# Kernel optimization log

Measured on AMD Instinct MI355X. Metric: run time of the kernel, lower is better.

## Reference

```python
import jax, jax.numpy as jnp
import numpy as np

LRELU_ALPHA = 0.2   # LeakyReLU negative slope (alpha init arg)
NEG_INF = -9e15     # masking constant used by standard GAT layers

B, N, NFEAT, NHID, NHEAD, NPRED = 16, 1024, 16, 32, 4, 12


def setup_inputs() -> dict:
    key = jax.random.key(0)
    ks = jax.random.split(key, 8)
    x = jax.random.normal(ks[0], (B, N, NFEAT), dtype=jnp.float32)
    adj = jax.random.randint(ks[1], (N, N), 0, 2, dtype=jnp.int32)
    s = 0.1
    W = jax.random.normal(ks[2], (NHEAD, NFEAT, NHID), dtype=jnp.float32) * s
    a_src = jax.random.normal(ks[3], (NHEAD, NHID), dtype=jnp.float32) * s
    a_dst = jax.random.normal(ks[4], (NHEAD, NHID), dtype=jnp.float32) * s
    W_out = jax.random.normal(ks[5], (NHEAD * NHID, NPRED), dtype=jnp.float32) * s
    a_out_src = jax.random.normal(ks[6], (NPRED,), dtype=jnp.float32) * s
    a_out_dst = jax.random.normal(ks[7], (NPRED,), dtype=jnp.float32) * s
    return {"x": x, "adj": adj, "W": W, "a_src": a_src, "a_dst": a_dst,
            "W_out": W_out, "a_out_src": a_out_src, "a_out_dst": a_out_dst}


def reference(x, adj, W, a_src, a_dst, W_out, a_out_src, a_out_dst):
    # Eval mode: all F.dropout calls are identity.
    mask = adj > 0  # [N, N], broadcast over batch (and heads)

    # --- multi-head GAT layer (concat=True), all heads vectorized ---
    Wh = jnp.einsum('bnf,hfk->bhnk', x, W)                 # [B,H,N,K]
    f_src = jnp.einsum('bhnk,hk->bhn', Wh, a_src)          # [B,H,N]
    f_dst = jnp.einsum('bhnk,hk->bhn', Wh, a_dst)
    e = jax.nn.leaky_relu(f_src[..., :, None] + f_dst[..., None, :], LRELU_ALPHA)
    attn = jax.nn.softmax(jnp.where(mask, e, NEG_INF), axis=-1)  # [B,H,N,N]
    h = jax.nn.elu(jnp.einsum('bhnm,bhmk->bhnk', attn, Wh))      # concat=True -> ELU
    b, H, n, k = h.shape
    h = jnp.transpose(h, (0, 2, 1, 3)).reshape(b, n, H * k)  # concat heads, dim=2

    # --- output GAT layer (concat=False) ---
    Wh2 = h @ W_out                                        # [B,N,npred]
    g_src = Wh2 @ a_out_src                                # [B,N]
    g_dst = Wh2 @ a_out_dst
    e2 = jax.nn.leaky_relu(g_src[:, :, None] + g_dst[:, None, :], LRELU_ALPHA)
    attn2 = jax.nn.softmax(jnp.where(mask, e2, NEG_INF), axis=-1)
    out = jax.nn.elu(jnp.einsum('bnm,bmp->bnp', attn2, Wh2))  # outer F.elu in STGAT
    return out.reshape(b, -1)                              # [B, N*npred]
```

## Files before the change

kernel.cpp:

```cpp
#include <hip/hip_runtime.h>
#include <cmath>

#define B_    16
#define N_    1024
#define NHID_ 32
#define NHEAD_ 4
#define NPRED_ 12
#define ALPHA 0.2f
#define LOG2E 1.442695041f

typedef __attribute__((ext_vector_type(8)))  short          short8;
typedef __attribute__((ext_vector_type(4)))  float          floatx4;
typedef __attribute__((ext_vector_type(2)))  float          float2v;
typedef __attribute__((ext_vector_type(4)))  unsigned       uintx4;
typedef __attribute__((ext_vector_type(4)))  unsigned short ushort4v;
typedef __attribute__((ext_vector_type(8)))  unsigned short ushort8v;

__device__ __forceinline__ float bs2f(unsigned short s) {
    return __uint_as_float(((unsigned)s) << 16);
}
__device__ __forceinline__ short f2bs(float f) {
    unsigned u = __float_as_uint(f);
    unsigned r = (u + 0x7fffu + ((u >> 16) & 1u)) >> 16;
    return (short)r;
}
__device__ __forceinline__ float ldin(const void* p, long i, int isbf) {
    if (isbf) return bs2f(((const unsigned short*)p)[i]);
    return ((const float*)p)[i];
}
__device__ __forceinline__ float fexp2(float x) {
#if __has_builtin(__builtin_amdgcn_exp2f)
    return __builtin_amdgcn_exp2f(x);
#else
    return __expf(x * 0.6931471805599453f);
#endif
}
__device__ __forceinline__ unsigned pk2t(unsigned u0, unsigned u1) {
#if __has_builtin(__builtin_amdgcn_perm)
    return __builtin_amdgcn_perm(u1, u0, 0x07060302u);
#else
    return (u0 >> 16) | (u1 & 0xffff0000u);
#endif
}
__device__ __forceinline__ float2v vmax2(float2v a, float2v b) {
#if __has_builtin(__builtin_elementwise_max)
    return __builtin_elementwise_max(a, b);
#else
    float2v r; r.x = fmaxf(a.x, b.x); r.y = fmaxf(a.y, b.y); return r;
#endif
}
__device__ __forceinline__ float2v vfma2(float2v a, float2v b, float2v c) {
#if __has_builtin(__builtin_elementwise_fma)
    return __builtin_elementwise_fma(a, b, c);
#else
    float2v r; r.x = __builtin_fmaf(a.x, b.x, c.x); r.y = __builtin_fmaf(a.y, b.y, c.y); return r;
#endif
}
__device__ __forceinline__ int detect_isbf(const unsigned short* xu) {
    int lane = threadIdx.x & 63;
    uint4 v = ((const uint4*)xu)[lane];
    unsigned wv[4] = {v.x, v.y, v.z, v.w};
    bool any = false;
#pragma unroll
    for (int i = 0; i < 4; ++i) {
        any |= (((wv[i] & 0xffffu) >> 7) & 0xffu) >= 160u;
        any |= (((wv[i] >> 16) >> 7) & 0xffu) >= 160u;
    }
    return __popcll(__ballot(any)) < 8;
}

__global__ __launch_bounds__(256) void k01_prep_wh(
    const unsigned short* __restrict__ xu, const int* __restrict__ adj,
    const void* __restrict__ x, const void* __restrict__ W,
    const void* __restrict__ a_src, const void* __restrict__ a_dst,
    unsigned short* __restrict__ bias,
    short* __restrict__ WhB, float* __restrict__ f_src, float* __restrict__ f_dst)
{
    int tid = threadIdx.x;
    if (blockIdx.x < 512) {
        int gid = blockIdx.x * 256 + tid;
        long base = (long)gid * 8;
        int4 a0 = *(const int4*)(adj + base);
        int4 a1 = *(const int4*)(adj + base + 4);
        uint4 wv;
        wv.x = (a0.x ? 0u : 0xFF80u) | (a0.y ? 0u : 0xFF800000u);
        wv.y = (a0.z ? 0u : 0xFF80u) | (a0.w ? 0u : 0xFF800000u);
        wv.z = (a1.x ? 0u : 0xFF80u) | (a1.y ? 0u : 0xFF800000u);
        wv.w = (a1.z ? 0u : 0xFF80u) | (a1.w ? 0u : 0xFF800000u);
        *(uint4*)(bias + base) = wv;
        return;
    }
    int isbf = detect_isbf(xu);
    __shared__ float Ws[16][32];
    __shared__ float xs[32][17];
    __shared__ float as_s[32], ad_s[32];
    __shared__ float Wa_s[16], Wad_s[16];
    int bid = blockIdx.x - 512;
    int bh = bid >> 5;
    int n0 = (bid & 31) * 32;
    int b  = bh >> 2, hh = bh & 3;

    if (!isbf) {
        const float* Wf = (const float*)W + hh * 512;
        if (tid < 128) {
            float4 v = *(const float4*)(Wf + tid * 4);
            int f = (tid * 4) >> 5, k = (tid * 4) & 31;
            Ws[f][k] = v.x; Ws[f][k+1] = v.y; Ws[f][k+2] = v.z; Ws[f][k+3] = v.w;
        }
        const float* xf = (const float*)x + ((long)(b * N_ + n0)) * 16;
        if (tid < 128) {
            float4 v = *(const float4*)(xf + tid * 4);
            int r = tid >> 2, f = (tid & 3) * 4;
            xs[r][f] = v.x; xs[r][f+1] = v.y; xs[r][f+2] = v.z; xs[r][f+3] = v.w;
        }
    } else {
        const unsigned short* Wb = (const unsigned short*)W + hh * 512;
        if (tid < 128) {
            ushort4v v = *(const ushort4v*)(Wb + tid * 4);
            int f = (tid * 4) >> 5, k = (tid * 4) & 31;
            Ws[f][k] = bs2f(v[0]); Ws[f][k+1] = bs2f(v[1]);
            Ws[f][k+2] = bs2f(v[2]); Ws[f][k+3] = bs2f(v[3]);
        }
        const unsigned short* xb = (const unsigned short*)x + ((long)(b * N_ + n0)) * 16;
        if (tid < 64) {
            ushort8v v = *(const ushort8v*)(xb + tid * 8);
            int r = tid >> 1, f = (tid & 1) * 8;
#pragma unroll
            for (int i = 0; i < 8; ++i) xs[r][f + i] = bs2f(v[i]);
        }
    }
    if (tid < 32) {
        as_s[tid] = ldin(a_src, hh * 32 + tid, isbf);
        ad_s[tid] = ldin(a_dst, hh * 32 + tid, isbf);
    }
    __syncthreads();

    if (tid < 32) {
        int f = tid & 15;
        const float* av = (tid < 16) ? as_s : ad_s;
        float s = 0.f;
#pragma unroll
        for (int kk = 0; kk < 32; ++kk) s += Ws[f][kk] * av[kk];
        ((tid < 16) ? Wa_s : Wad_s)[f] = s;
    }
    __syncthreads();

    if (tid < 32) {
        float fs = 0.f, fd = 0.f;
#pragma unroll
        for (int f = 0; f < 16; ++f) {
            fs += xs[tid][f] * Wa_s[f];
            fd += xs[tid][f] * Wad_s[f];
        }
        int n = n0 + tid;
        f_src[bh * N_ + n] = fs * LOG2E;
        f_dst[bh * N_ + n] = fd * LOG2E;
    }

    int k = tid & 31, rb = tid >> 5;
#pragma unroll
    for (int it = 0; it < 4; ++it) {
        int r = it * 8 + rb;
        float acc = 0.f;
#pragma unroll
        for (int f = 0; f < 16; ++f) acc += xs[r][f] * Ws[f][k];
        int n = n0 + r;
        int kstep = n >> 5, quad = (n >> 3) & 3, jj = n & 7;
        int t = k >> 4, l = quad * 16 + (k & 15);
        WhB[((((size_t)bh * 32 + kstep) * 2 + t) * 64 + l) * 8 + jj] = f2bs(acc);
    }
}

__global__ __launch_bounds__(256) void k2_attn1(
    const float* __restrict__ f_src, const float* __restrict__ f_dst,
    const unsigned short* __restrict__ bias, const short* __restrict__ WhB,
    unsigned short* __restrict__ h2)
{
    __shared__ float fdst_s[N_];
    __shared__ float wmax[4];
    __shared__ float Sh[4][16];
    int bid = blockIdx.x;
    int xcd = bid & 7, j = bid >> 3;
    int bh = j & 63;
    int tile = xcd + 8 * (j >> 6);
    int tid = threadIdx.x;
    int w = tid >> 6, lane = tid & 63;

    float lmax = -INFINITY;
    for (int idx = tid; idx < N_; idx += 256) {
        float v = f_dst[bh * N_ + idx];
        fdst_s[idx] = v;
        lmax = fmaxf(lmax, v);
    }
#pragma unroll
    for (int m = 32; m; m >>= 1) lmax = fmaxf(lmax, __shfl_xor(lmax, m, 64));
    if (lane == 0) wmax[w] = lmax;
    __syncthreads();
    float maxfd = fmaxf(fmaxf(wmax[0], wmax[1]), fmaxf(wmax[2], wmax[3]));

    int i0 = tile * 64 + w * 16;
    int r = lane & 15, q = lane >> 4;

    float fsr = f_src[bh * N_ + i0 + r];
    float Mv = fsr + maxfd;
    float M = fmaxf(Mv, ALPHA * Mv);
    float2v a1v; a1v.x = fsr - M;          a1v.y = a1v.x;
    float2v a2v; a2v.x = ALPHA * fsr - M;  a2v.y = a2v.x;
    float2v alv; alv.x = ALPHA;            alv.y = ALPHA;
    float2v s2 = {};

    floatx4 acc0 = {}, acc1 = {};
    const unsigned short* brow = bias + (size_t)(i0 + r) * N_ + q * 8;
    const float* fdp = fdst_s + q * 8;
    const short* wb = WhB + (((size_t)bh * 64) * 64 + lane) * 8;

    uint4  bu_n = *(const uint4*)(brow);
    short8 w0_n = *(const short8*)(wb);
    short8 w1_n = *(const short8*)(wb + 512);

#pragma unroll 4
    for (int kk = 0; kk < 32; ++kk) {
        uint4 bu = bu_n;
        short8 bfr0 = w0_n, bfr1 = w1_n;
        if (kk < 31) {
            bu_n = *(const uint4*)(brow + (kk + 1) * 32);
            w0_n = *(const short8*)(wb + (kk + 1) * 1024);
            w1_n = *(const short8*)(wb + (kk + 1) * 1024 + 512);
        }
        float4 fda = *(const float4*)(fdp + kk * 32);
        float4 fdb = *(const float4*)(fdp + kk * 32 + 4);
        unsigned bw[4] = {bu.x, bu.y, bu.z, bu.w};
        float fdx[8] = {fda.x, fda.y, fda.z, fda.w, fdb.x, fdb.y, fdb.z, fdb.w};
        unsigned dpk[4];
#pragma unroll
        for (int p = 0; p < 4; ++p) {
            float2v fd2; fd2.x = fdx[2 * p]; fd2.y = fdx[2 * p + 1];
            float2v b2;  b2.x = __uint_as_float(bw[p] << 16);
                         b2.y = __uint_as_float(bw[p] & 0xffff0000u);
            float2v t1 = a1v + fd2;
            float2v t2 = vfma2(alv, fd2, a2v);
            float2v arg = vmax2(t1, t2) + b2;
            float2v pv; pv.x = fexp2(arg.x); pv.y = fexp2(arg.y);
            s2 += pv;
            dpk[p] = pk2t(__float_as_uint(pv.x), __float_as_uint(pv.y));
        }
        uintx4 du; du[0] = dpk[0]; du[1] = dpk[1]; du[2] = dpk[2]; du[3] = dpk[3];
        short8 afr = __builtin_bit_cast(short8, du);
        acc0 = __builtin_amdgcn_mfma_f32_16x16x32_bf16(afr, bfr0, acc0, 0, 0, 0);
        acc1 = __builtin_amdgcn_mfma_f32_16x16x32_bf16(afr, bfr1, acc1, 0, 0, 0);
    }

    float s = s2.x + s2.y;
    s += __shfl_xor(s, 16, 64);
    s += __shfl_xor(s, 32, 64);
    if (lane < 16) Sh[w][lane] = s;
    __builtin_amdgcn_wave_barrier();

    int bb = bh >> 2, head = bh & 3;
#pragma unroll
    for (int reg = 0; reg < 4; ++reg) {
        int row = q * 4 + reg;
        float rsv = 1.f / Sh[w][row];
        unsigned short* hrow = &h2[((size_t)(bb * N_ + i0 + row)) * 128 + head * 32];
        float v0 = acc0[reg] * rsv;
        v0 = v0 > 0.f ? v0 : expm1f(v0);
        hrow[r]      = (unsigned short)f2bs(v0);
        float v1 = acc1[reg] * rsv;
        v1 = v1 > 0.f ? v1 : expm1f(v1);
        hrow[16 + r] = (unsigned short)f2bs(v1);
    }
}

__global__ __launch_bounds__(256) void k3_out_proj(
    const unsigned short* __restrict__ xu,
    const unsigned short* __restrict__ h2, const void* __restrict__ W_out,
    const void* __restrict__ a_out_src, const void* __restrict__ a_out_dst,
    short* __restrict__ Wh2B, float* __restrict__ g_src, float* __restrict__ g_dst)
{
    int isbf = detect_isbf(xu);
    __shared__ float WoT[16][132];
    __shared__ float hs[16][132];
    __shared__ float aos[16], aod[16];
    int bid = blockIdx.x;
    int b = bid >> 6;
    int n0 = (bid & 63) * 16;
    int tid = threadIdx.x;

    if (!isbf) {
        const float* Wf = (const float*)W_out;
        for (int idx = tid; idx < 384; idx += 256) {
            float4 v = *(const float4*)(Wf + idx * 4);
            float vv[4] = {v.x, v.y, v.z, v.w};
#pragma unroll
            for (int i = 0; i < 4; ++i) {
                int e = idx * 4 + i;
                WoT[e % NPRED_][e / NPRED_] = vv[i];
            }
        }
    } else {
        const unsigned short* Wb = (const unsigned short*)W_out;
        for (int idx = tid; idx < 192; idx += 256) {
            ushort8v v = *(const ushort8v*)(Wb + idx * 8);
#pragma unroll
            for (int i = 0; i < 8; ++i) {
                int e = idx * 8 + i;
                WoT[e % NPRED_][e / NPRED_] = bs2f(v[i]);
            }
        }
    }
    if (tid < 128) {
#pragma unroll
        for (int p = NPRED_; p < 16; ++p) WoT[p][tid] = 0.f;
    }
    if (tid < 16) {
        aos[tid] = (tid < NPRED_) ? ldin(a_out_src, tid, isbf) : 0.f;
        aod[tid] = (tid < NPRED_) ? ldin(a_out_dst, tid, isbf) : 0.f;
    }
    {
        ushort8v v = *(const ushort8v*)(h2 + ((size_t)(b * N_ + n0 + (tid >> 4))) * 128 + (tid & 15) * 8);
        int r = tid >> 4, c8 = (tid & 15) * 8;
#pragma unroll
        for (int i = 0; i < 8; ++i) hs[r][c8 + i] = bs2f(v[i]);
    }
    __syncthreads();

    int r = tid >> 4, p = tid & 15;
    float acc = 0.f;
#pragma unroll 8
    for (int c4 = 0; c4 < 128; c4 += 4) {
        float4 hv = *(const float4*)&hs[r][c4];
        float4 wv = *(const float4*)&WoT[p][c4];
        acc += hv.x * wv.x + hv.y * wv.y + hv.z * wv.z + hv.w * wv.w;
    }

    float t1 = acc * aos[p], t2 = acc * aod[p];
#pragma unroll
    for (int m = 8; m; m >>= 1) {
        t1 += __shfl_xor(t1, m, 64);
        t2 += __shfl_xor(t2, m, 64);
    }
    int n = n0 + r;
    if (p == 0) {
        g_src[b * N_ + n] = t1 * LOG2E;
        g_dst[b * N_ + n] = t2 * LOG2E;
    }
    int kstep = n >> 5, quad = (n >> 3) & 3, jj = n & 7;
    short val = (p == 15) ? (short)0x3F80 : f2bs(acc);
    Wh2B[(((size_t)b * 32 + kstep) * 64 + quad * 16 + p) * 8 + jj] = val;
}

__global__ __launch_bounds__(256) void k4_attn2(
    const unsigned short* __restrict__ xu,
    const float* __restrict__ g_src, const float* __restrict__ g_dst,
    const unsigned short* __restrict__ bias, const short* __restrict__ Wh2B,
    void* __restrict__ out)
{
    int isbf = detect_isbf(xu);
    __shared__ float gdst_s[N_];
    __shared__ float wmax[4];
    __shared__ float xch[3][64][4];
    int bid = blockIdx.x;
    int xcd = bid & 7, j = bid >> 3;
    int b = j & 15;
    int tile = xcd + 8 * (j >> 4);
    int tid = threadIdx.x;
    int ch = tid >> 6, lane = tid & 63;

    float lmax = -INFINITY;
    for (int idx = tid; idx < N_; idx += 256) {
        float v = g_dst[b * N_ + idx];
        gdst_s[idx] = v;
        lmax = fmaxf(lmax, v);
    }
#pragma unroll
    for (int m = 32; m; m >>= 1) lmax = fmaxf(lmax, __shfl_xor(lmax, m, 64));
    if (lane == 0) wmax[ch] = lmax;
    __syncthreads();
    float maxgd = fmaxf(fmaxf(wmax[0], wmax[1]), fmaxf(wmax[2], wmax[3]));

    int i0 = tile * 16;
    int r = lane & 15, q = lane >> 4;

    float gsr = g_src[b * N_ + i0 + r];
    float Mv = gsr + maxgd;
    float M = fmaxf(Mv, ALPHA * Mv);
    float2v a1v; a1v.x = gsr - M;          a1v.y = a1v.x;
    float2v a2v; a2v.x = ALPHA * gsr - M;  a2v.y = a2v.x;
    float2v alv; alv.x = ALPHA;            alv.y = ALPHA;

    floatx4 acc = {};
    const unsigned short* brow = bias + (size_t)(i0 + r) * N_ + ch * 256 + q * 8;
    const float* fdp = gdst_s + ch * 256 + q * 8;
    const short* wb = Wh2B + (((size_t)b * 32 + ch * 8) * 64 + lane) * 8;

    uint4  bu_n = *(const uint4*)(brow);
    short8 wf_n = *(const short8*)(wb);

#pragma unroll 4
    for (int kk = 0; kk < 8; ++kk) {
        uint4 bu = bu_n;
        short8 bfr = wf_n;
        if (kk < 7) {
            bu_n = *(const uint4*)(brow + (kk + 1) * 32);
            wf_n = *(const short8*)(wb + (kk + 1) * 512);
        }
        float4 fda = *(const float4*)(fdp + kk * 32);
        float4 fdb = *(const float4*)(fdp + kk * 32 + 4);
        unsigned bw[4] = {bu.x, bu.y, bu.z, bu.w};
        float fdx[8] = {fda.x, fda.y, fda.z, fda.w, fdb.x, fdb.y, fdb.z, fdb.w};
        unsigned dpk[4];
#pragma unroll
        for (int p = 0; p < 4; ++p) {
            float2v fd2; fd2.x = fdx[2 * p]; fd2.y = fdx[2 * p + 1];
            float2v b2;  b2.x = __uint_as_float(bw[p] << 16);
                         b2.y = __uint_as_float(bw[p] & 0xffff0000u);
            float2v t1 = a1v + fd2;
            float2v t2 = vfma2(alv, fd2, a2v);
            float2v arg = vmax2(t1, t2) + b2;
            float2v pv; pv.x = fexp2(arg.x); pv.y = fexp2(arg.y);
            dpk[p] = pk2t(__float_as_uint(pv.x), __float_as_uint(pv.y));
        }
        uintx4 du; du[0] = dpk[0]; du[1] = dpk[1]; du[2] = dpk[2]; du[3] = dpk[3];
        short8 afr = __builtin_bit_cast(short8, du);
        acc = __builtin_amdgcn_mfma_f32_16x16x32_bf16(afr, bfr, acc, 0, 0, 0);
    }

    if (ch != 0) {
#pragma unroll
        for (int i = 0; i < 4; ++i) xch[ch - 1][lane][i] = acc[i];
    }
    __syncthreads();
    if (ch == 0) {
#pragma unroll
        for (int t = 0; t < 3; ++t)
#pragma unroll
            for (int i = 0; i < 4; ++i) acc[i] += xch[t][lane][i];
        int srclane = (lane & 48) + 15;
#pragma unroll
        for (int reg = 0; reg < 4; ++reg) {
            int row = q * 4 + reg;
            float Srow = __shfl(acc[reg], srclane, 64);
            float v = acc[reg] / Srow;
            float o = v > 0.f ? v : expm1f(v);
            if (r < NPRED_) {
                size_t idx = (size_t)b * (N_ * NPRED_) + (size_t)(i0 + row) * NPRED_ + r;
                if (isbf) ((unsigned short*)out)[idx] = (unsigned short)f2bs(o);
                else      ((float*)out)[idx] = o;
            }
        }
    }
}

extern "C" void kernel_launch(void* const* d_in, const int* in_sizes, int n_in,
                              void* d_out, int out_size, void* d_ws, size_t ws_size,
                              hipStream_t stream)
{
    (void)in_sizes; (void)n_in; (void)out_size; (void)ws_size;
    const void* x      = d_in[0];
    const int*  adj    = (const int*)d_in[1];
    const void* W      = d_in[2];
    const void* a_src  = d_in[3];
    const void* a_dst  = d_in[4];
    const void* W_out  = d_in[5];
    const void* a_osrc = d_in[6];
    const void* a_odst = d_in[7];
    const unsigned short* xu = (const unsigned short*)x;

    char* ws = (char*)d_ws;
    short* WhB   = (short*)(ws);
    float* f_src = (float*)(ws + (4 << 20));
    float* f_dst = (float*)(ws + (4 << 20) + (256 << 10));
    unsigned short* h2 = (unsigned short*)(ws + (4 << 20) + (512 << 10));
    short* Wh2B  = (short*)(ws + (12 << 20) + (512 << 10));
    float* g_src = (float*)(ws + (13 << 20));
    float* g_dst = (float*)(ws + (13 << 20) + (64 << 10));
    unsigned short* bias = (unsigned short*)(ws + (14 << 20));

    hipLaunchKernelGGL(k01_prep_wh, dim3(2560), dim3(256), 0, stream,
                       xu, adj, x, W, a_src, a_dst, bias, WhB, f_src, f_dst);
    hipLaunchKernelGGL(k2_attn1,    dim3(1024), dim3(256), 0, stream,
                       f_src, f_dst, bias, WhB, h2);
    hipLaunchKernelGGL(k3_out_proj, dim3(1024), dim3(256), 0, stream,
                       xu, h2, W_out, a_osrc, a_odst, Wh2B, g_src, g_dst);
    hipLaunchKernelGGL(k4_attn2,    dim3(1024), dim3(256), 0, stream,
                       xu, g_src, g_dst, bias, Wh2B, d_out);
}
```

Baseline: 121.1 us.

## Process two 16-row groups per wave in attention kernel to reuse WhB fragments

```diff
diff --git a/kernel.cpp b/kernel.cpp
--- a/kernel.cpp
+++ b/kernel.cpp
@@ -67,6 +67,37 @@
         any |= (((wv[i] >> 16) >> 7) & 0xffu) >= 160u;
     }
     return __popcll(__ballot(any)) < 8;
+}
+
+struct SGrp {
+    float2v a1v, a2v;
+    float2v s2;
+};
+__device__ __forceinline__ void sg_init(SGrp& g, float fsr, float maxfd) {
+    float Mv = fsr + maxfd;
+    float M = fmaxf(Mv, ALPHA * Mv);
+    g.a1v.x = fsr - M;         g.a1v.y = g.a1v.x;
+    g.a2v.x = ALPHA * fsr - M; g.a2v.y = g.a2v.x;
+    g.s2.x = 0.f; g.s2.y = 0.f;
+}
+__device__ __forceinline__ short8 sg_frag(SGrp& g, const unsigned bw[4],
+                                          const float fdx[8]) {
+    float2v alv; alv.x = ALPHA; alv.y = ALPHA;
+    unsigned dpk[4];
+#pragma unroll
+    for (int p = 0; p < 4; ++p) {
+        float2v fd2; fd2.x = fdx[2 * p]; fd2.y = fdx[2 * p + 1];
+        float2v b2;  b2.x = __uint_as_float(bw[p] << 16);
+                     b2.y = __uint_as_float(bw[p] & 0xffff0000u);
+        float2v t1 = g.a1v + fd2;
+        float2v t2 = vfma2(alv, fd2, g.a2v);
+        float2v arg = vmax2(t1, t2) + b2;
+        float2v pv; pv.x = fexp2(arg.x); pv.y = fexp2(arg.y);
+        g.s2 += pv;
+        dpk[p] = pk2t(__float_as_uint(pv.x), __float_as_uint(pv.y));
+    }
+    uintx4 du; du[0] = dpk[0]; du[1] = dpk[1]; du[2] = dpk[2]; du[3] = dpk[3];
+    return __builtin_bit_cast(short8, du);
 }
 
 __global__ __launch_bounds__(256) void k01_prep_wh(
@@ -178,11 +209,10 @@
 {
     __shared__ float fdst_s[N_];
     __shared__ float wmax[4];
-    __shared__ float Sh[4][16];
+    __shared__ float Sh[4][32];
     int bid = blockIdx.x;
-    int xcd = bid & 7, j = bid >> 3;
-    int bh = j & 63;
-    int tile = xcd + 8 * (j >> 6);
+    int tile = bid & 7;
+    int bh = bid >> 3;
     int tid = threadIdx.x;
     int w = tid >> 6, lane = tid & 63;
 
@@ -198,76 +228,80 @@
     __syncthreads();
     float maxfd = fmaxf(fmaxf(wmax[0], wmax[1]), fmaxf(wmax[2], wmax[3]));
 
-    int i0 = tile * 64 + w * 16;
+    int i0 = tile * 128 + w * 32;
     int r = lane & 15, q = lane >> 4;
 
-    float fsr = f_src[bh * N_ + i0 + r];
-    float Mv = fsr + maxfd;
-    float M = fmaxf(Mv, ALPHA * Mv);
-    float2v a1v; a1v.x = fsr - M;          a1v.y = a1v.x;
-    float2v a2v; a2v.x = ALPHA * fsr - M;  a2v.y = a2v.x;
-    float2v alv; alv.x = ALPHA;            alv.y = ALPHA;
-    float2v s2 = {};
-
-    floatx4 acc0 = {}, acc1 = {};
-    const unsigned short* brow = bias + (size_t)(i0 + r) * N_ + q * 8;
+    SGrp gA, gB;
+    sg_init(gA, f_src[bh * N_ + i0 + r],      maxfd);
+    sg_init(gB, f_src[bh * N_ + i0 + 16 + r], maxfd);
+
+    floatx4 acc0A = {}, acc1A = {}, acc0B = {}, acc1B = {};
+    const unsigned short* browA = bias + (size_t)(i0 + r) * N_ + q * 8;
+    const unsigned short* browB = browA + (size_t)16 * N_;
     const float* fdp = fdst_s + q * 8;
     const short* wb = WhB + (((size_t)bh * 64) * 64 + lane) * 8;
 
-    uint4  bu_n = *(const uint4*)(brow);
+    uint4  buA_n = *(const uint4*)(browA);
+    uint4  buB_n = *(const uint4*)(browB);
     short8 w0_n = *(const short8*)(wb);
     short8 w1_n = *(const short8*)(wb + 512);
 
-#pragma unroll 4
+#pragma unroll 2
     for (int kk = 0; kk < 32; ++kk) {
-        uint4 bu = bu_n;
+        uint4 buA = buA_n, buB = buB_n;
         short8 bfr0 = w0_n, bfr1 = w1_n;
         if (kk < 31) {
-            bu_n = *(const uint4*)(brow + (kk + 1) * 32);
+            buA_n = *(const uint4*)(browA + (kk + 1) * 32);
+            buB_n = *(const uint4*)(browB + (kk + 1) * 32);
             w0_n = *(const short8*)(wb + (kk + 1) * 1024);
             w1_n = *(const short8*)(wb + (kk + 1) * 1024 + 512);
         }
         float4 fda = *(const float4*)(fdp + kk * 32);
         float4 fdb = *(const float4*)(fdp + kk * 32 + 4);
-        unsigned bw[4] = {bu.x, bu.y, bu.z, bu.w};
         float fdx[8] = {fda.x, fda.y, fda.z, fda.w, fdb.x, fdb.y, fdb.z, fdb.w};
-        unsigned dpk[4];
-#pragma unroll
-        for (int p = 0; p < 4; ++p) {
-            float2v fd2; fd2.x = fdx[2 * p]; fd2.y = fdx[2 * p + 1];
-            float2v b2;  b2.x = __uint_as_float(bw[p] << 16);
-                         b2.y = __uint_as_float(bw[p] & 0xffff0000u);
-            float2v t1 = a1v + fd2;
-            float2v t2 = vfma2(alv, fd2, a2v);
-            float2v arg = vmax2(t1, t2) + b2;
-            float2v pv; pv.x = fexp2(arg.x); pv.y = fexp2(arg.y);
-            s2 += pv;
-            dpk[p] = pk2t(__float_as_uint(pv.x), __float_as_uint(pv.y));
-        }
-        uintx4 du; du[0] = dpk[0]; du[1] = dpk[1]; du[2] = dpk[2]; du[3] = dpk[3];
-        short8 afr = __builtin_bit_cast(short8, du);
-        acc0 = __builtin_amdgcn_mfma_f32_16x16x32_bf16(afr, bfr0, acc0, 0, 0, 0);
-        acc1 = __builtin_amdgcn_mfma_f32_16x16x32_bf16(afr, bfr1, acc1, 0, 0, 0);
-    }
-
-    float s = s2.x + s2.y;
-    s += __shfl_xor(s, 16, 64);
-    s += __shfl_xor(s, 32, 64);
-    if (lane < 16) Sh[w][lane] = s;
+        unsigned bwA[4] = {buA.x, buA.y, buA.z, buA.w};
+        unsigned bwB[4] = {buB.x, buB.y, buB.z, buB.w};
+        short8 afrA = sg_frag(gA, bwA, fdx);
+        short8 afrB = sg_frag(gB, bwB, fdx);
+        acc0A = __builtin_amdgcn_mfma_f32_16x16x32_bf16(afrA, bfr0, acc0A, 0, 0, 0);
+        acc1A = __builtin_amdgcn_mfma_f32_16x16x32_bf16(afrA, bfr1, acc1A, 0, 0, 0);
+        acc0B = __builtin_amdgcn_mfma_f32_16x16x32_bf16(afrB, bfr0, acc0B, 0, 0, 0);
+        acc1B = __builtin_amdgcn_mfma_f32_16x16x32_bf16(afrB, bfr1, acc1B, 0, 0, 0);
+    }
+
+    float sA = gA.s2.x + gA.s2.y;
+    sA += __shfl_xor(sA, 16, 64);
+    sA += __shfl_xor(sA, 32, 64);
+    float sB = gB.s2.x + gB.s2.y;
+    sB += __shfl_xor(sB, 16, 64);
+    sB += __shfl_xor(sB, 32, 64);
+    if (lane < 16) { Sh[w][lane] = sA; Sh[w][16 + lane] = sB; }
     __builtin_amdgcn_wave_barrier();
 
     int bb = bh >> 2, head = bh & 3;
 #pragma unroll
     for (int reg = 0; reg < 4; ++reg) {
         int row = q * 4 + reg;
-        float rsv = 1.f / Sh[w][row];
-        unsigned short* hrow = &h2[((size_t)(bb * N_ + i0 + row)) * 128 + head * 32];
-        float v0 = acc0[reg] * rsv;
-        v0 = v0 > 0.f ? v0 : expm1f(v0);
-        hrow[r]      = (unsigned short)f2bs(v0);
-        float v1 = acc1[reg] * rsv;
-        v1 = v1 > 0.f ? v1 : expm1f(v1);
-        hrow[16 + r] = (unsigned short)f2bs(v1);
+        {
+            float rsv = 1.f / Sh[w][row];
+            unsigned short* hrow = &h2[((size_t)(bb * N_ + i0 + row)) * 128 + head * 32];
+            float v0 = acc0A[reg] * rsv;
+            v0 = v0 > 0.f ? v0 : expm1f(v0);
+            hrow[r]      = (unsigned short)f2bs(v0);
+            float v1 = acc1A[reg] * rsv;
+            v1 = v1 > 0.f ? v1 : expm1f(v1);
+            hrow[16 + r] = (unsigned short)f2bs(v1);
+        }
+        {
+            float rsv = 1.f / Sh[w][16 + row];
+            unsigned short* hrow = &h2[((size_t)(bb * N_ + i0 + 16 + row)) * 128 + head * 32];
+            float v0 = acc0B[reg] * rsv;
+            v0 = v0 > 0.f ? v0 : expm1f(v0);
+            hrow[r]      = (unsigned short)f2bs(v0);
+            float v1 = acc1B[reg] * rsv;
+            v1 = v1 > 0.f ? v1 : expm1f(v1);
+            hrow[16 + r] = (unsigned short)f2bs(v1);
+        }
     }
 }
 
@@ -478,7 +512,7 @@
 
     hipLaunchKernelGGL(k01_prep_wh, dim3(2560), dim3(256), 0, stream,
                        xu, adj, x, W, a_src, a_dst, bias, WhB, f_src, f_dst);
-    hipLaunchKernelGGL(k2_attn1,    dim3(1024), dim3(256), 0, stream,
+    hipLaunchKernelGGL(k2_attn1,    dim3(512),  dim3(256), 0, stream,
                        f_src, f_dst, bias, WhB, h2);
     hipLaunchKernelGGL(k3_out_proj, dim3(1024), dim3(256), 0, stream,
                        xu, h2, W_out, a_osrc, a_odst, Wh2B, g_src, g_dst);
```

After: 116.6 us. 3.7% less time.
